# Optimization experiments

Hardware: AMD Instinct MI355X
Metric: run time of the kernel (lower is better)

Reference implementation:

```python
import jax, jax.numpy as jnp
import numpy as np

B, L, F, H = 1024, 256, 128, 256
A, CH, OUT = 128, 256, 512


def setup_inputs() -> dict:
    key = jax.random.key(0)
    ks = jax.random.split(key, 12)
    s = lambda k, shape, fan: (jax.random.normal(k, shape, jnp.float32) / np.float32(np.sqrt(fan)))
    return dict(
        input_batch=jax.random.normal(ks[0], (B, L, F), jnp.float32),
        tte=jax.random.randint(ks[1], (B,), 0, L, jnp.int32),
        W_ih=s(ks[2], (3 * H, F), F), W_hh=s(ks[3], (3 * H, H), H),
        b_ih=jnp.zeros((3 * H,), jnp.float32), b_hh=jnp.zeros((3 * H,), jnp.float32),
        W_out=s(ks[4], (F, H), H), b_out=jnp.zeros((F,), jnp.float32),
        Wa=s(ks[5], (H, A), H), Ua=s(ks[6], (F, A), F), va=s(ks[7], (A,), A),
        W1=s(ks[8], (H + F, CH), H + F), b1=jnp.zeros((CH,), jnp.float32),
        W2=s(ks[9], (CH, OUT), CH), b2=jnp.zeros((OUT,), jnp.float32),
    )


def _gru_step(x, h, W_ih, W_hh, b_ih, b_hh):
    # torch.nn.GRU single-step math, batched over B
    gi = x @ W_ih.T + b_ih          # [B,3H]
    gh = h @ W_hh.T + b_hh          # [B,3H]
    i_r, i_z, i_n = jnp.split(gi, 3, axis=-1)
    h_r, h_z, h_n = jnp.split(gh, 3, axis=-1)
    r = jax.nn.sigmoid(i_r + h_r)
    z = jax.nn.sigmoid(i_z + h_z)
    n = jnp.tanh(i_n + r * h_n)
    return (1.0 - z) * n + z * h


def reference(input_batch, tte, W_ih, W_hh, b_ih, b_hh, W_out, b_out,
              Wa, Ua, va, W1, b1, W2, b2):
    Bn, Ln, Fn = input_batch.shape
    Hn = W_hh.shape[1]
    h0 = jnp.zeros((Bn, Hn), input_batch.dtype)
    xs = jnp.moveaxis(input_batch, 1, 0)  # [L,B,F]
    ts = jnp.arange(Ln)

    def step(h, inp):
        x_t, t = inp
        h_new = _gru_step(x_t, h, W_ih, W_hh, b_ih, b_hh)
        active = (t < tte)[:, None]          # ragged length mask [B,1]
        h = jnp.where(active, h_new, h)      # freeze state past tte
        out_t = jnp.where(active, h_new @ W_out.T + b_out, 0.0)
        hid_t = jnp.where(active, h_new, 0.0)
        return h, (out_t, hid_t)

    _, (outs, hids) = jax.lax.scan(step, h0, (xs, ts))
    output_batch = jnp.moveaxis(outs, 0, 1)   # [B,L,F], zero-padded like the torch code
    hidden_vec = jnp.moveaxis(hids, 0, 1)     # [B,L,H], zero-padded

    # last measurement at index tte (the torch code indexes batch[tte])
    last = jnp.take_along_axis(input_batch, tte[:, None, None].astype(jnp.int32), axis=1)[:, 0]  # [B,F]

    # decoder: additive attention over the full padded trajectory
    scores = jnp.tanh(hidden_vec @ Wa + (last @ Ua)[:, None, :]) @ va   # [B,L]
    alpha = jax.nn.softmax(scores, axis=-1)
    context = jnp.einsum('bl,blh->bh', alpha, hidden_vec)               # [B,H]

    # causes network: MLP + softmax over cause x time-bin grid
    zc = jax.nn.relu(jnp.concatenate([context, last], axis=-1) @ W1 + b1)
    fht = jax.nn.softmax(zc @ W2 + b2, axis=-1)                         # [B,OUT]
    return output_batch, fht
```

## Files before the change

### kernel.cpp

```cpp
#include <hip/hip_runtime.h>

#define B_ 1024
#define L_ 256
#define F_ 128
#define H_ 256

typedef __bf16 bf16x8 __attribute__((ext_vector_type(8)));
typedef __bf16 bf16x4 __attribute__((ext_vector_type(4)));
typedef float f32x4 __attribute__((ext_vector_type(4)));
typedef int i32x4 __attribute__((ext_vector_type(4)));

#define MFMA16(a, b, c) __builtin_amdgcn_mfma_f32_16x16x32_bf16((a), (b), (c), 0, 0, 0)
#define MFMA_I8(a, b, c) __builtin_amdgcn_mfma_i32_16x16x64_i8((a), (b), (c), 0, 0, 0)
#define BAR_LDS() asm volatile("s_waitcnt lgkmcnt(0)\n\ts_barrier" ::: "memory")

__device__ __forceinline__ float rcp_f(float x) { return __builtin_amdgcn_rcpf(x); }
__device__ __forceinline__ float sigm(float x) { return rcp_f(1.f + __expf(-x)); }
__device__ __forceinline__ float tanh_f(float x) {
  float ax = fabsf(x);
  float e = __expf(-2.f * ax);
  float r = (1.f - e) * rcp_f(1.f + e);
  return copysignf(r, x);
}
__device__ __forceinline__ bf16x8 ld8(const __bf16* p) { return *(const bf16x8*)p; }
__device__ __forceinline__ float wave_max(float v) {
#pragma unroll
  for (int d = 1; d < 64; d <<= 1) v = fmaxf(v, __shfl_xor(v, d));
  return v;
}
__device__ __forceinline__ float wave_sum(float v) {
#pragma unroll
  for (int d = 1; d < 64; d <<= 1) v += __shfl_xor(v, d);
  return v;
}
__device__ __forceinline__ unsigned pack4(float a, float b, float c, float d, float inv) {
  return (unsigned)(unsigned char)(signed char)__float2int_rn(a * inv)
       | ((unsigned)(unsigned char)(signed char)__float2int_rn(b * inv) << 8)
       | ((unsigned)(unsigned char)(signed char)__float2int_rn(c * inv) << 16)
       | ((unsigned)(unsigned char)(signed char)__float2int_rn(d * inv) << 24);
}

__global__ void cvt_kernel(const float* __restrict__ wih_f, const float* __restrict__ wa_f,
                           const float* __restrict__ ua_f, const float* __restrict__ w1_f,
                           const float* __restrict__ w2_f,
                           __bf16* __restrict__ wih, __bf16* __restrict__ wa_t,
                           __bf16* __restrict__ ua_t, __bf16* __restrict__ w1_t,
                           __bf16* __restrict__ w2_t) {
  int i = blockIdx.x * 256 + threadIdx.x;
  if (i < 98304) wih[i] = (__bf16)wih_f[i];
  else if (i < 131072) {
    int j = i - 98304; int a = j >> 8, k = j & 255;
    wa_t[j] = (__bf16)wa_f[k * 128 + a];
  } else if (i < 147456) {
    int j = i - 131072; int a = j >> 7, f = j & 127;
    ua_t[j] = (__bf16)ua_f[f * 128 + a];
  } else if (i < 245760) {
    int j = i - 147456; int c = j / 384, k = j - c * 384;
    w1_t[j] = (__bf16)w1_f[k * 256 + c];
  } else if (i < 376832) {
    int j = i - 245760; int o = j >> 8, k = j & 255;
    w2_t[j] = (__bf16)w2_f[k * 512 + o];
  }
}

__global__ void quant_kernel(const float* __restrict__ whh_f, const float* __restrict__ wout_f,
                             signed char* __restrict__ wqg_f,
                             signed char* __restrict__ wqo_f,
                             float* __restrict__ dq) {
  const int c = blockIdx.x * 256 + threadIdx.x;
  if (c >= 896) return;
  const float* row = (c < 768) ? whh_f + (size_t)c * 256 : wout_f + (size_t)(c - 768) * 256;
  float m = 0.f;
  for (int k4 = 0; k4 < 64; ++k4) {
    float4 v = *(const float4*)(row + k4 * 4);
    m = fmaxf(m, fmaxf(fmaxf(fabsf(v.x), fabsf(v.y)), fmaxf(fabsf(v.z), fabsf(v.w))));
  }
  const float inv = (m > 1e-30f) ? 127.f / m : 0.f;
  dq[c] = m / 16129.f;
  if (c < 768) {
    const int g = c >> 8, cc = c & 255;
    const int t16 = cc >> 4, l15q = cc & 15;
    for (int kt = 0; kt < 4; ++kt)
      for (int lgq = 0; lgq < 4; ++lgq) {
        signed char* dst = wqg_f + (size_t)((((g * 16 + t16) * 4 + kt) * 64) + lgq * 16 + l15q) * 16;
        const float* src = row + kt * 64 + lgq * 16;
        for (int j4 = 0; j4 < 4; ++j4) {
          float4 v = *(const float4*)(src + j4 * 4);
          *(unsigned*)(dst + j4 * 4) = pack4(v.x, v.y, v.z, v.w, inv);
        }
      }
  } else {
    const int oc = c - 768;
    const int t8 = oc >> 4, l15q = oc & 15;
    for (int kt = 0; kt < 4; ++kt)
      for (int lgq = 0; lgq < 4; ++lgq) {
        signed char* dst = wqo_f + (size_t)(((t8 * 4 + kt) * 64) + lgq * 16 + l15q) * 16;
        const float* src = row + kt * 64 + lgq * 16;
        for (int j4 = 0; j4 < 4; ++j4) {
          float4 v = *(const float4*)(src + j4 * 4);
          *(unsigned*)(dst + j4 * 4) = pack4(v.x, v.y, v.z, v.w, inv);
        }
      }
  }
}

__global__ __launch_bounds__(512, 2) void gi_gemm_kernel(
    const float* __restrict__ x, const float* __restrict__ b_ih,
    const float* __restrict__ b_hh, const __bf16* __restrict__ wih,
    const int* __restrict__ tte, __bf16* __restrict__ gi,
    float* __restrict__ out) {
  const int tid = threadIdx.x;
  const int lane = tid & 63, w = tid >> 6;
  const int l15 = lane & 15, lg = lane >> 4, kofs = lg * 8;
  const int bblk = blockIdx.x & 63, tgrp = blockIdx.x >> 6;
  const int b0 = bblk * 16;

  {
    const int pr = tid >> 1, ph = tid & 1;
    const int bl = pr >> 4, tl = pr & 15;
    const int bb = b0 + bl, tt = tgrp * 16 + tl;
    if (tt >= tte[bb]) {
      float4* dst = (float4*)(out + ((size_t)bb * L_ + tt) * F_) + ph * 16;
#pragma unroll
      for (int i = 0; i < 16; ++i) dst[i] = float4{0.f, 0.f, 0.f, 0.f};
    }
  }

  int tmaxB = 0;
  for (int i = 0; i < 16; ++i) tmaxB = max(tmaxB, tte[b0 + i]);
  if (tgrp * 16 > tmaxB) return;

  bf16x8 wf[6][4];
  float bias[6];
#pragma unroll
  for (int tile = 0; tile < 6; ++tile) {
    const int gate = tile >> 1;
    const int c = w * 32 + (tile & 1) * 16 + l15;
    const int col = gate * 256 + c;
#pragma unroll
    for (int kt = 0; kt < 4; ++kt) wf[tile][kt] = ld8(wih + (size_t)col * 128 + kt * 32 + kofs);
    bias[tile] = (gate == 0) ? b_ih[c] + b_hh[c]
               : (gate == 1) ? b_ih[256 + c] + b_hh[256 + c]
                             : b_ih[512 + c];
  }

#pragma unroll 1
  for (int ti = 0; ti < 16; ++ti) {
    const int t = tgrp * 16 + ti;
    if (t > tmaxB) break;
    const float* xb = x + ((size_t)(b0 + l15) * L_ + t) * F_ + kofs;
    bf16x8 xfr[4];
#pragma unroll
    for (int kt = 0; kt < 4; ++kt) {
      float4 a = *(const float4*)(xb + kt * 32);
      float4 b = *(const float4*)(xb + kt * 32 + 4);
      xfr[kt][0] = (__bf16)a.x; xfr[kt][1] = (__bf16)a.y;
      xfr[kt][2] = (__bf16)a.z; xfr[kt][3] = (__bf16)a.w;
      xfr[kt][4] = (__bf16)b.x; xfr[kt][5] = (__bf16)b.y;
      xfr[kt][6] = (__bf16)b.z; xfr[kt][7] = (__bf16)b.w;
    }
    f32x4 acc[6];
#pragma unroll
    for (int tile = 0; tile < 6; ++tile) {
      acc[tile][0] = bias[tile]; acc[tile][1] = bias[tile];
      acc[tile][2] = bias[tile]; acc[tile][3] = bias[tile];
    }
#pragma unroll
    for (int kt = 0; kt < 4; ++kt)
#pragma unroll
      for (int tile = 0; tile < 6; ++tile)
        acc[tile] = MFMA16(xfr[kt], wf[tile][kt], acc[tile]);

    const size_t chunk = (((size_t)t * 64 + bblk) * 8 + w) * 6;
#pragma unroll
    for (int tile = 0; tile < 6; ++tile) {
      bf16x4 pk;
      pk[0] = (__bf16)acc[tile][0]; pk[1] = (__bf16)acc[tile][1];
      pk[2] = (__bf16)acc[tile][2]; pk[3] = (__bf16)acc[tile][3];
      *(bf16x4*)(gi + (chunk + tile) * 256 + (lg * 16 + l15) * 4) = pk;
    }
  }
}

__global__ __launch_bounds__(1024) void gru256_kernel(
    const int* __restrict__ tte, const float* __restrict__ b_hh,
    const signed char* __restrict__ wqg_f, const signed char* __restrict__ wqo_f,
    const float* __restrict__ dq, const __bf16* __restrict__ gi,
    const float* __restrict__ b_out,
    __bf16* __restrict__ hid, float* __restrict__ out) {
  __shared__ signed char hb[2][4][288];
  __shared__ f32x4 raccP[4][260];
  const int tid = threadIdx.x;
  const int lane = tid & 63, w = tid >> 6;
  const int l15 = lane & 15, lg = lane >> 4;
  const int blk = blockIdx.x;
  const int b0 = blk * 4;

  for (int i = tid; i < 2 * 4 * 288; i += 1024) ((signed char*)hb)[i] = 0;

  const int colL = w * 16 + l15;
  i32x4 wR[4], wZ[4], wN[4];
#pragma unroll
  for (int kt = 0; kt < 4; ++kt) {
    wR[kt] = *(const i32x4*)(wqg_f + (size_t)((((0 * 16 + w) * 4 + kt) * 64) + lane) * 16);
    wZ[kt] = *(const i32x4*)(wqg_f + (size_t)((((1 * 16 + w) * 4 + kt) * 64) + lane) * 16);
    wN[kt] = *(const i32x4*)(wqg_f + (size_t)((((2 * 16 + w) * 4 + kt) * 64) + lane) * 16);
  }
  const int ocol = (w & 7) * 16 + l15;
  i32x4 ow[4];
#pragma unroll
  for (int kt = 0; kt < 4; ++kt)
    ow[kt] = *(const i32x4*)(wqo_f + (size_t)(((w & 7) * 4 + kt) * 64 + lane) * 16);
  const float dqo = dq[768 + ocol];
  const float bo = b_out[ocol];
  int tteO[4];
#pragma unroll
  for (int r = 0; r < 4; ++r) tteO[r] = tte[b0 + r];
  float* outp = out + ((size_t)b0 * L_) * F_ + ocol;

  const int grow = tid >> 8, gcol = tid & 255;
  const float dqR = dq[gcol], dqZ = dq[256 + gcol], dqN = dq[512 + gcol];
  const float bhn = b_hh[512 + gcol];
  const int tteL = tte[b0 + grow];
  int tmax = 0;
#pragma unroll
  for (int i = 0; i < 4; ++i) tmax = max(tmax, tte[b0 + i]);

  const size_t gb0 = (((size_t)(blk >> 2) * 8 + (gcol >> 5)) * 6 + ((gcol >> 4) & 1)) * 256
                   + (size_t)((blk & 3) * 16 + (gcol & 15)) * 4 + grow;
  const __bf16* gp = gi + gb0;
  __bf16 gRn = gp[0], gZn = gp[512], gNn = gp[1024];
  const __bf16* gpp = gp + 786432;

  __bf16* hidp = hid + ((size_t)(b0 + grow) * L_) * H_ + gcol;
  float hprev = 0.f;

  __syncthreads();

#pragma unroll 1
  for (int t = 0; t < tmax; ++t) {
    const int c = t & 1, nc = c ^ 1;

    const float grf = (float)gRn, gzf = (float)gZn, gnf = (float)gNn;
    gRn = gpp[0]; gZn = gpp[512]; gNn = gpp[1024];
    if (t < 254) gpp += 786432;

    i32x4 aR = {0, 0, 0, 0}, aZ = {0, 0, 0, 0}, aN = {0, 0, 0, 0}, ac = {0, 0, 0, 0};
#pragma unroll
    for (int kt = 0; kt < 4; ++kt) {
      const i32x4 hA = *(const i32x4*)&hb[c][l15 & 3][kt * 64 + lg * 16];
      aR = MFMA_I8(hA, wR[kt], aR);
      aZ = MFMA_I8(hA, wZ[kt], aZ);
      aN = MFMA_I8(hA, wN[kt], aN);
      if (w < 8) ac = MFMA_I8(hA, ow[kt], ac);
    }
    if (w < 8 && t > 0) {
      if (lg == 0) {
#pragma unroll
        for (int r = 0; r < 4; ++r)
          if (t - 1 < tteO[r]) outp[(size_t)r * (L_ * F_)] = (float)ac[r] * dqo + bo;
      }
      outp += F_;
    }
    if (lg == 0) {
#pragma unroll
      for (int r = 0; r < 4; ++r) {
        f32x4 v = {(float)aR[r], (float)aZ[r], (float)aN[r], 0.f};
        raccP[r][colL] = v;
      }
    }
    BAR_LDS();

    {
      const f32x4 rv = raccP[grow][gcol];
      const float rg = sigm(grf + rv[0] * dqR);
      const float zg = sigm(gzf + rv[1] * dqZ);
      const float ng = tanh_f(gnf + rg * (rv[2] * dqN + bhn));
      const float hnew = zg * (hprev - ng) + ng;
      const float hw = (t < tteL) ? hnew : hprev;
      hprev = hw;
      hb[nc][grow][gcol] = (signed char)__float2int_rn(hw * 127.f);
      if (t < tteL) *hidp = (__bf16)hw;
      hidp += H_;
    }
    BAR_LDS();
  }

  if (w < 8 && tmax > 0) {
    const int cf = tmax & 1;
    i32x4 ac = {0, 0, 0, 0};
#pragma unroll
    for (int kt = 0; kt < 4; ++kt) {
      const i32x4 hA = *(const i32x4*)&hb[cf][l15 & 3][kt * 64 + lg * 16];
      ac = MFMA_I8(hA, ow[kt], ac);
    }
    if (lg == 0) {
#pragma unroll
      for (int r = 0; r < 4; ++r)
        if (tmax - 1 < tteO[r]) outp[(size_t)r * (L_ * F_)] = (float)ac[r] * dqo + bo;
    }
  }
}

__global__ __launch_bounds__(512, 2) void decoder3_kernel(
    const float* __restrict__ x, const int* __restrict__ tte,
    const __bf16* __restrict__ hid, const __bf16* __restrict__ wa_t,
    const __bf16* __restrict__ ua_t, const __bf16* __restrict__ w1_t,
    const __bf16* __restrict__ w2_t, const float* __restrict__ va,
    const float* __restrict__ b1, const float* __restrict__ b2,
    float* __restrict__ fht) {
  __shared__ __bf16 catb[16][392];
  __shared__ float u_s[4][128];
  __shared__ float sa[4][256];
  __shared__ __bf16 z1b[16][264];
  __shared__ float lg2[4][516];
  __shared__ float ctxp[2][4][256];
  __shared__ float va_s[128];
  __shared__ int tte_s[4];
  const int tid = threadIdx.x;
  const int lane = tid & 63, w = tid >> 6;
  const int l15 = lane & 15, lg = lane >> 4, kofs = lg * 8;
  const int b0 = blockIdx.x * 4;

  if (tid < 4) tte_s[tid] = tte[b0 + tid];
  if (tid < 128) va_s[tid] = va[tid];
  if (tid < 392)
    for (int r = 4; r < 16; ++r) catb[r][tid] = (__bf16)0.f;
  if (tid < 264)
    for (int r = 4; r < 16; ++r) z1b[r][tid] = (__bf16)0.f;
  __syncthreads();

  {
    const int row = tid >> 7, c = tid & 127;
    catb[row][256 + c] = (__bf16)x[((size_t)(b0 + row) * L_ + tte_s[row]) * F_ + c];
  }
  __syncthreads();

  {
    f32x4 uacc = {0, 0, 0, 0};
#pragma unroll
    for (int kt = 0; kt < 4; ++kt) {
      const bf16x8 af = *(const bf16x8*)&catb[l15][256 + kt * 32 + kofs];
      const bf16x8 bf = ld8(ua_t + (size_t)(w * 16 + l15) * 128 + kt * 32 + kofs);
      uacc = MFMA16(af, bf, uacc);
    }
#pragma unroll
    for (int r = 0; r < 4; ++r) {
      const int row = 4 * lg + r;
      if (row < 4) u_s[row][w * 16 + l15] = uacc[r];
    }
  }
  __syncthreads();

  bf16x8 zero8;
#pragma unroll
  for (int j = 0; j < 8; ++j) zero8[j] = (__bf16)0.f;
#pragma unroll 1
  for (int it = 0; it < 8; ++it) {
    const int pair = it * 8 + w;
    const int b = pair >> 4, mtile = pair & 15;
    const int tteB = tte_s[b];
    const int trow = mtile * 16 + l15;
    const __bf16* hrow = hid + ((size_t)(b0 + b) * L_ + trow) * H_ + kofs;
    bf16x8 af[8];
#pragma unroll
    for (int kt = 0; kt < 8; ++kt) af[kt] = (trow < tteB) ? ld8(hrow + kt * 32) : zero8;
    f32x4 sacc[8];
#pragma unroll
    for (int ct = 0; ct < 8; ++ct) { sacc[ct][0] = 0; sacc[ct][1] = 0; sacc[ct][2] = 0; sacc[ct][3] = 0; }
#pragma unroll
    for (int kt = 0; kt < 8; ++kt)
#pragma unroll
      for (int ct = 0; ct < 8; ++ct)
        sacc[ct] = MFMA16(af[kt], ld8(wa_t + (size_t)(ct * 16 + l15) * 256 + kt * 32 + kofs), sacc[ct]);
    float sp[4] = {0, 0, 0, 0};
#pragma unroll
    for (int ct = 0; ct < 8; ++ct) {
      const int a = ct * 16 + l15;
      const float ua = u_s[b][a], vv = va_s[a];
#pragma unroll
      for (int r = 0; r < 4; ++r) sp[r] += tanh_f(sacc[ct][r] + ua) * vv;
    }
#pragma unroll
    for (int r = 0; r < 4; ++r) {
      sp[r] += __shfl_xor(sp[r], 1);
      sp[r] += __shfl_xor(sp[r], 2);
      sp[r] += __shfl_xor(sp[r], 4);
      sp[r] += __shfl_xor(sp[r], 8);
    }
    if (l15 == 0) {
#pragma unroll
      for (int r = 0; r < 4; ++r) sa[b][mtile * 16 + 4 * lg + r] = sp[r];
    }
  }
  __syncthreads();

  if (w < 4) {
    float sv[4];
#pragma unroll
    for (int j = 0; j < 4; ++j) sv[j] = sa[w][lane + 64 * j];
    float mx = fmaxf(fmaxf(sv[0], sv[1]), fmaxf(sv[2], sv[3]));
    mx = wave_max(mx);
    float es[4], ss = 0.f;
#pragma unroll
    for (int j = 0; j < 4; ++j) { es[j] = __expf(sv[j] - mx); ss += es[j]; }
    ss = wave_sum(ss);
    const float inv = rcp_f(ss);
#pragma unroll
    for (int j = 0; j < 4; ++j) sa[w][lane + 64 * j] = es[j] * inv;
  }
  __syncthreads();

  {
    const int be = w & 3, half = w >> 2;
    const int tteE = tte_s[be];
    float c4[4] = {0.f, 0.f, 0.f, 0.f};
    const __bf16* hp = hid + ((size_t)(b0 + be) * L_ + half) * H_ + lane * 4;
#pragma unroll 2
    for (int t = half; t < tteE; t += 2) {
      const float al = sa[be][t];
      const bf16x4 hv = *(const bf16x4*)hp;
      hp += 2 * H_;
#pragma unroll
      for (int j = 0; j < 4; ++j) c4[j] += al * (float)hv[j];
    }
#pragma unroll
    for (int j = 0; j < 4; ++j) ctxp[half][be][lane * 4 + j] = c4[j];
  }
  __syncthreads();
  if (w < 4) {
#pragma unroll
    for (int j = 0; j < 4; ++j)
      catb[w][lane * 4 + j] = (__bf16)(ctxp[0][w][lane * 4 + j] + ctxp[1][w][lane * 4 + j]);
  }
  __syncthreads();

#pragma unroll 1
  for (int half = 0; half < 2; ++half) {
    const int nt = w * 2 + half;
    f32x4 zacc = {0, 0, 0, 0};
#pragma unroll
    for (int kt = 0; kt < 12; ++kt) {
      const bf16x8 af = *(const bf16x8*)&catb[l15][kt * 32 + kofs];
      const bf16x8 bf = ld8(w1_t + (size_t)(nt * 16 + l15) * 384 + kt * 32 + kofs);
      zacc = MFMA16(af, bf, zacc);
    }
    const float bb = b1[nt * 16 + l15];
#pragma unroll
    for (int r = 0; r < 4; ++r) {
      const int row = 4 * lg + r;
      if (row < 4) z1b[row][nt * 16 + l15] = (__bf16)fmaxf(zacc[r] + bb, 0.f);
    }
  }
  __syncthreads();

#pragma unroll 1
  for (int q = 0; q < 4; ++q) {
    const int nt = w * 4 + q;
    f32x4 oacc = {0, 0, 0, 0};
#pragma unroll
    for (int kt = 0; kt < 8; ++kt) {
      const bf16x8 af = *(const bf16x8*)&z1b[l15][kt * 32 + kofs];
      const bf16x8 bf = ld8(w2_t + (size_t)(nt * 16 + l15) * 256 + kt * 32 + kofs);
      oacc = MFMA16(af, bf, oacc);
    }
    const float bb = b2[nt * 16 + l15];
#pragma unroll
    for (int r = 0; r < 4; ++r) {
      const int row = 4 * lg + r;
      if (row < 4) lg2[row][nt * 16 + l15] = oacc[r] + bb;
    }
  }
  __syncthreads();
  if (w < 4) {
    float lv[8];
    float mx = -1e30f;
#pragma unroll
    for (int j = 0; j < 8; ++j) { lv[j] = lg2[w][lane + 64 * j]; mx = fmaxf(mx, lv[j]); }
    mx = wave_max(mx);
    float s2 = 0.f;
#pragma unroll
    for (int j = 0; j < 8; ++j) { lv[j] = __expf(lv[j] - mx); s2 += lv[j]; }
    s2 = wave_sum(s2);
    const float inv2 = rcp_f(s2);
#pragma unroll
    for (int j = 0; j < 8; ++j)
      fht[(size_t)(b0 + w) * 512 + lane + 64 * j] = lv[j] * inv2;
  }
}

extern "C" void kernel_launch(void* const* d_in, const int* in_sizes, int n_in,
                              void* d_out, int out_size, void* d_ws, size_t ws_size,
                              hipStream_t stream) {
  const float* x = (const float*)d_in[0];
  const int* tte = (const int*)d_in[1];
  const float* W_ih = (const float*)d_in[2];
  const float* W_hh = (const float*)d_in[3];
  const float* b_ih = (const float*)d_in[4];
  const float* b_hh = (const float*)d_in[5];
  const float* W_out = (const float*)d_in[6];
  const float* b_out = (const float*)d_in[7];
  const float* Wa = (const float*)d_in[8];
  const float* Ua = (const float*)d_in[9];
  const float* va = (const float*)d_in[10];
  const float* W1 = (const float*)d_in[11];
  const float* b1 = (const float*)d_in[12];
  const float* W2 = (const float*)d_in[13];
  const float* b2 = (const float*)d_in[14];

  char* ws = (char*)d_ws;
  __bf16* wih = (__bf16*)(ws + 0);
  __bf16* wa_t = (__bf16*)(ws + 196608);
  __bf16* ua_t = (__bf16*)(ws + 262144);
  __bf16* w1_t = (__bf16*)(ws + 294912);
  __bf16* w2_t = (__bf16*)(ws + 491520);
  signed char* wqg_f = (signed char*)(ws + 753664);
  signed char* wqo_f = (signed char*)(ws + 950272);
  float* dq = (float*)(ws + 983040);
  __bf16* hid = (__bf16*)(ws + 1048576);
  __bf16* gi = (__bf16*)(ws + 135266304);

  float* out = (float*)d_out;
  float* fht = out + (size_t)33554432;

  cvt_kernel<<<1472, 256, 0, stream>>>(W_ih, Wa, Ua, W1, W2,
                                       wih, wa_t, ua_t, w1_t, w2_t);
  quant_kernel<<<4, 256, 0, stream>>>(W_hh, W_out, wqg_f, wqo_f, dq);
  gi_gemm_kernel<<<1024, 512, 0, stream>>>(x, b_ih, b_hh, wih, tte, gi, out);
  gru256_kernel<<<256, 1024, 0, stream>>>(tte, b_hh, wqg_f, wqo_f, dq, gi,
                                          b_out, hid, out);
  decoder3_kernel<<<256, 512, 0, stream>>>(x, tte, hid, wa_t, ua_t, w1_t, w2_t,
                                           va, b1, b2, fht);
}
```

Measured before the change: 749.6 us.

## Replace LDS gate-accumulator exchange with intra-wave shuffles, drop one barrier

Each wave now finishes the gate nonlinearity for its own 16 columns across the 4 batch rows, instead of staging the MFMA accumulators through shared memory and re-reading them under a different thread mapping. Lane ownership is remapped so each lane takes row lane>>4 and column w*16+(lane&15), and the accumulator values are fetched with 12 cross-lane shuffles. This removes the shared raccP buffer and one block-wide barrier per timestep from the serial recurrence. The cost is the shuffle traffic and a different global access pattern for the gi loads and hid stores.

```diff
diff --git a/kernel.cpp b/kernel.cpp
--- a/kernel.cpp
+++ b/kernel.cpp
@@ -189,7 +189,6 @@
     const float* __restrict__ b_out,
     __bf16* __restrict__ hid, float* __restrict__ out) {
   __shared__ signed char hb[2][4][288];
-  __shared__ f32x4 raccP[4][260];
   const int tid = threadIdx.x;
   const int lane = tid & 63, w = tid >> 6;
   const int l15 = lane & 15, lg = lane >> 4;
@@ -198,7 +197,6 @@
 
   for (int i = tid; i < 2 * 4 * 288; i += 1024) ((signed char*)hb)[i] = 0;
 
-  const int colL = w * 16 + l15;
   i32x4 wR[4], wZ[4], wN[4];
 #pragma unroll
   for (int kt = 0; kt < 4; ++kt) {
@@ -218,21 +216,21 @@
   for (int r = 0; r < 4; ++r) tteO[r] = tte[b0 + r];
   float* outp = out + ((size_t)b0 * L_) * F_ + ocol;
 
-  const int grow = tid >> 8, gcol = tid & 255;
-  const float dqR = dq[gcol], dqZ = dq[256 + gcol], dqN = dq[512 + gcol];
-  const float bhn = b_hh[512 + gcol];
-  const int tteL = tte[b0 + grow];
+  const int groww = lane >> 4, gcolw = w * 16 + (lane & 15);
+  const float dqR = dq[gcolw], dqZ = dq[256 + gcolw], dqN = dq[512 + gcolw];
+  const float bhn = b_hh[512 + gcolw];
+  const int tteL = tte[b0 + groww];
   int tmax = 0;
 #pragma unroll
   for (int i = 0; i < 4; ++i) tmax = max(tmax, tte[b0 + i]);
 
-  const size_t gb0 = (((size_t)(blk >> 2) * 8 + (gcol >> 5)) * 6 + ((gcol >> 4) & 1)) * 256
-                   + (size_t)((blk & 3) * 16 + (gcol & 15)) * 4 + grow;
+  const size_t gb0 = (((size_t)(blk >> 2) * 8 + (gcolw >> 5)) * 6 + ((gcolw >> 4) & 1)) * 256
+                   + (size_t)((blk & 3) * 16 + (gcolw & 15)) * 4 + groww;
   const __bf16* gp = gi + gb0;
   __bf16 gRn = gp[0], gZn = gp[512], gNn = gp[1024];
   const __bf16* gpp = gp + 786432;
 
-  __bf16* hidp = hid + ((size_t)(b0 + grow) * L_) * H_ + gcol;
+  __bf16* hidp = hid + ((size_t)(b0 + groww) * L_) * H_ + gcolw;
   float hprev = 0.f;
 
   __syncthreads();
@@ -262,24 +260,26 @@
       }
       outp += F_;
     }
-    if (lg == 0) {
-#pragma unroll
-      for (int r = 0; r < 4; ++r) {
-        f32x4 v = {(float)aR[r], (float)aZ[r], (float)aN[r], 0.f};
-        raccP[r][colL] = v;
-      }
-    }
-    BAR_LDS();
 
     {
-      const f32x4 rv = raccP[grow][gcol];
-      const float rg = sigm(grf + rv[0] * dqR);
-      const float zg = sigm(gzf + rv[1] * dqZ);
-      const float ng = tanh_f(gnf + rg * (rv[2] * dqN + bhn));
+      const int srcl = lane & 15;
+      int tR0 = __shfl(aR[0], srcl), tR1 = __shfl(aR[1], srcl);
+      int tR2 = __shfl(aR[2], srcl), tR3 = __shfl(aR[3], srcl);
+      int tZ0 = __shfl(aZ[0], srcl), tZ1 = __shfl(aZ[1], srcl);
+      int tZ2 = __shfl(aZ[2], srcl), tZ3 = __shfl(aZ[3], srcl);
+      int tN0 = __shfl(aN[0], srcl), tN1 = __shfl(aN[1], srcl);
+      int tN2 = __shfl(aN[2], srcl), tN3 = __shfl(aN[3], srcl);
+      const int vR = groww == 0 ? tR0 : groww == 1 ? tR1 : groww == 2 ? tR2 : tR3;
+      const int vZ = groww == 0 ? tZ0 : groww == 1 ? tZ1 : groww == 2 ? tZ2 : tZ3;
+      const int vN = groww == 0 ? tN0 : groww == 1 ? tN1 : groww == 2 ? tN2 : tN3;
+
+      const float rg = sigm(grf + (float)vR * dqR);
+      const float zg = sigm(gzf + (float)vZ * dqZ);
+      const float ng = tanh_f(gnf + rg * ((float)vN * dqN + bhn));
       const float hnew = zg * (hprev - ng) + ng;
       const float hw = (t < tteL) ? hnew : hprev;
       hprev = hw;
-      hb[nc][grow][gcol] = (signed char)__float2int_rn(hw * 127.f);
+      hb[nc][groww][gcolw] = (signed char)__float2int_rn(hw * 127.f);
       if (t < tteL) *hidp = (__bf16)hw;
       hidp += H_;
     }
```

After: 711.5 us. 1.05x faster.
